# Optimization experiments

Hardware: AMD Instinct MI355X
Metric: run time of the kernel (lower is better)

The kernel has to match this reference:

```python
import jax, jax.numpy as jnp
import numpy as np

N = 10000
E = 160000
DIMS = [256, 256, 256, 256]
EPS = 1e-5
DSCALE = 1.0
SPE_IDX = 0


def setup_inputs() -> dict:
    key = jax.random.key(0)
    ks = jax.random.split(key, 40)
    inp = {}
    inp['x'] = jax.random.normal(ks[0], (N, DIMS[0]), dtype=jnp.float32)
    inp['src'] = jax.random.randint(ks[1], (E,), 0, N, dtype=jnp.int32)
    inp['dst'] = jax.random.randint(ks[2], (E,), 0, N, dtype=jnp.int32)
    k = 3
    for i, (din, dout) in enumerate(zip(DIMS[:-1], DIMS[1:])):
        s = 1.0 / np.sqrt(din)
        inp[f'Ws{i}'] = jax.random.uniform(ks[k], (din, dout), jnp.float32, -s, s); k += 1
        inp[f'Wn{i}'] = jax.random.uniform(ks[k], (din, dout), jnp.float32, -s, s); k += 1
        inp[f'b{i}'] = jnp.zeros((dout,), jnp.float32)
        inp[f'g{i}'] = jnp.ones((dout,), jnp.float32)
        inp[f'be{i}'] = jnp.zeros((dout,), jnp.float32)
    return inp


def _sage(h, src, dst, Ws, Wn, b):
    # mean aggregation over in-neighbors: segment-sum gathered src feats over dst
    agg = jax.ops.segment_sum(h[src], dst, num_segments=N)          # [N, din]
    deg = jax.ops.segment_sum(jnp.ones((E,), h.dtype), dst, num_segments=N)
    mean = agg / jnp.maximum(deg, 1.0)[:, None]
    return h @ Ws + mean @ Wn + b


def _bn(h, g, be):
    # BatchNorm1d, training mode (biased batch variance)
    mu = jnp.mean(h, axis=0)
    var = jnp.mean((h - mu) ** 2, axis=0)
    return (h - mu) * jax.lax.rsqrt(var + EPS) * g + be


def reference(x, src, dst, Ws0, Wn0, b0, g0, be0, Ws1, Wn1, b1, g1, be1,
              Ws2, Wn2, b2, g2, be2):
    params = [(Ws0, Wn0, b0, g0, be0), (Ws1, Wn1, b1, g1, be1),
              (Ws2, Wn2, b2, g2, be2)]
    n_layers = len(params)
    outs = x
    for i, (Ws, Wn, b, g, be) in enumerate(params):
        outs = _sage(outs, src, dst, Ws, Wn, b)
        # hid side-outputs (sigmoid(outs*dscale)[spe_idx]) don't affect outs path
        outs = _bn(outs, g, be)
        if i != n_layers - 1:
            outs = jax.nn.relu(outs)
        else:
            outs = jax.nn.sigmoid(outs)
    return outs
```

## Files before the change

### kernel.cpp

```cpp
#include <hip/hip_runtime.h>
#include <math.h>

#define NN 10000
#define EE 160000
#define DIM 256
#define KK 512
#define CAP 128
#define EPS_BN 1e-5f
#define AST 516

typedef __attribute__((ext_vector_type(8)))  short bf16x8;
typedef __attribute__((ext_vector_type(16))) float f32x16;

union U16 { uint2 u2[2]; bf16x8 v; };

static __device__ __forceinline__ unsigned short f2bf(float f) {
    unsigned u = __float_as_uint(f);
    unsigned r = (u + 0x7fffu + ((u >> 16) & 1u)) >> 16;
    return (unsigned short)r;
}
static __device__ __forceinline__ float bflo(unsigned v) { return __uint_as_float(v << 16); }
static __device__ __forceinline__ float bfhi(unsigned v) { return __uint_as_float(v & 0xffff0000u); }
static __device__ __forceinline__ unsigned packbf(float a, float b) {
    return (unsigned)f2bf(a) | ((unsigned)f2bf(b) << 16);
}

struct Params {
    const float* x; const int* src; const int* dst;
    const float *Ws0, *Wn0, *Ws1, *Wn1, *Ws2, *Wn2;
    const float *g0, *be0, *g1, *be1, *g2, *be2;
    float* out;
    unsigned short* hx;
    unsigned short* z0;
    unsigned short* z1;
    unsigned short* wcat;
    float* stats;
    int* cnt;
    int* slots;
};

static __device__ __forceinline__ void accum8(float* a, uint4 v) {
    a[0] += bflo(v.x); a[1] += bfhi(v.x);
    a[2] += bflo(v.y); a[3] += bfhi(v.y);
    a[4] += bflo(v.z); a[5] += bfhi(v.z);
    a[6] += bflo(v.w); a[7] += bfhi(v.w);
}
static __device__ __forceinline__ void accum8n(float* a, uint4 v,
                                               const float* sc, const float* sh) {
    a[0] += fmaxf(bflo(v.x) * sc[0] + sh[0], 0.f);
    a[1] += fmaxf(bfhi(v.x) * sc[1] + sh[1], 0.f);
    a[2] += fmaxf(bflo(v.y) * sc[2] + sh[2], 0.f);
    a[3] += fmaxf(bfhi(v.y) * sc[3] + sh[3], 0.f);
    a[4] += fmaxf(bflo(v.z) * sc[4] + sh[4], 0.f);
    a[5] += fmaxf(bfhi(v.z) * sc[5] + sh[5], 0.f);
    a[6] += fmaxf(bflo(v.w) * sc[6] + sh[6], 0.f);
    a[7] += fmaxf(bfhi(v.w) * sc[7] + sh[7], 0.f);
}

__global__ __launch_bounds__(256) void k_prep(Params P) {
    int g0 = blockIdx.x * 256 + threadIdx.x;
    int stride = gridDim.x * 256;
    for (int g = g0; g < NN * 64; g += stride) {
        int r = g >> 6, c4 = (g & 63) * 4;
        float4 v = *(const float4*)(P.x + (size_t)r * DIM + c4);
        uint2 p; p.x = packbf(v.x, v.y); p.y = packbf(v.z, v.w);
        *(uint2*)(P.hx + (size_t)r * DIM + c4) = p;
    }
    for (int g = g0; g < 3 * DIM * KK; g += stride) {
        int L = g >> 17; int i = g & 131071;
        int k = i >> 8, n = i & 255;
        const float* Ws = (L == 0) ? P.Ws0 : ((L == 1) ? P.Ws1 : P.Ws2);
        const float* Wn = (L == 0) ? P.Wn0 : ((L == 1) ? P.Wn1 : P.Wn2);
        float v = (k < DIM) ? Ws[(size_t)k * DIM + n] : Wn[(size_t)(k - DIM) * DIM + n];
        P.wcat[(size_t)L * DIM * KK + (size_t)n * KK + k] = f2bf(v);
    }
    for (int g = g0; g < NN + 6 * DIM; g += stride) {
        if (g < NN) P.cnt[g] = 0;
        else P.stats[g - NN] = 0.f;
    }
}

__global__ __launch_bounds__(256) void k_bucket(Params P) {
    int e = blockIdx.x * 256 + threadIdx.x;
    if (e < EE) {
        int d = P.dst[e];
        int p = atomicAdd(&P.cnt[d], 1);
        if (p < CAP) P.slots[(size_t)d * CAP + p] = P.src[e];
    }
}

__global__ __launch_bounds__(512) void k_ag(Params P, int L,
                                            const unsigned short* __restrict__ gsrc,
                                            unsigned short* __restrict__ gdst) {
    __shared__ unsigned short At[32][AST];
    int t = threadIdx.x;
    int wave = t >> 6, lane = t & 63;
    int h = lane >> 5, l = lane & 31;

    float sc[8], sh[8];
    if (L > 0) {
        const float* st = P.stats + (L - 1) * 2 * DIM;
        const float* gam = (L == 1) ? P.g0 : P.g1;
        const float* bet = (L == 1) ? P.be0 : P.be1;
#pragma unroll
        for (int i = 0; i < 8; ++i) {
            int c = l * 8 + i;
            float mu  = st[c] * (1.0f / NN);
            float var = st[DIM + c] * (1.0f / NN) - mu * mu;
            float k = rsqrtf(var + EPS_BN) * gam[c];
            sc[i] = k;
            sh[i] = bet[c] - mu * k;
        }
    }
    const uint4* srcm = (const uint4*)gsrc;

    for (int i = 0; i < 4; ++i) {
        int m = wave * 4 + i;
        int node = blockIdx.x * 32 + m;
        unsigned short* arow = &At[m][0];
        if (node >= NN) {
            if (h == 0) {
                uint2 z2 = make_uint2(0u, 0u);
                *(uint2*)(arow + l * 8)           = z2;
                *(uint2*)(arow + l * 8 + 4)       = z2;
                *(uint2*)(arow + 256 + l * 8)     = z2;
                *(uint2*)(arow + 256 + l * 8 + 4) = z2;
            }
            continue;
        }
        int cnt = P.cnt[node]; if (cnt > CAP) cnt = CAP;
        const int* sl = P.slots + (size_t)node * CAP;
        if (h == 0) {
            uint4 z = srcm[(size_t)node * 32 + l];
            uint4 o;
            if (L > 0) {
                o.x = packbf(fmaxf(bflo(z.x) * sc[0] + sh[0], 0.f),
                             fmaxf(bfhi(z.x) * sc[1] + sh[1], 0.f));
                o.y = packbf(fmaxf(bflo(z.y) * sc[2] + sh[2], 0.f),
                             fmaxf(bfhi(z.y) * sc[3] + sh[3], 0.f));
                o.z = packbf(fmaxf(bflo(z.z) * sc[4] + sh[4], 0.f),
                             fmaxf(bfhi(z.z) * sc[5] + sh[5], 0.f));
                o.w = packbf(fmaxf(bflo(z.w) * sc[6] + sh[6], 0.f),
                             fmaxf(bfhi(z.w) * sc[7] + sh[7], 0.f));
            } else o = z;
            *(uint2*)(arow + l * 8)     = make_uint2(o.x, o.y);
            *(uint2*)(arow + l * 8 + 4) = make_uint2(o.z, o.w);
        }
        float a[8] = {0, 0, 0, 0, 0, 0, 0, 0};
        int j = h;
        if (L == 0) {
            for (; j + 6 < cnt; j += 8) {
                uint4 v0 = srcm[(size_t)sl[j + 0] * 32 + l];
                uint4 v1 = srcm[(size_t)sl[j + 2] * 32 + l];
                uint4 v2 = srcm[(size_t)sl[j + 4] * 32 + l];
                uint4 v3 = srcm[(size_t)sl[j + 6] * 32 + l];
                accum8(a, v0); accum8(a, v1); accum8(a, v2); accum8(a, v3);
            }
            for (; j < cnt; j += 2) accum8(a, srcm[(size_t)sl[j] * 32 + l]);
        } else {
            for (; j + 6 < cnt; j += 8) {
                uint4 v0 = srcm[(size_t)sl[j + 0] * 32 + l];
                uint4 v1 = srcm[(size_t)sl[j + 2] * 32 + l];
                uint4 v2 = srcm[(size_t)sl[j + 4] * 32 + l];
                uint4 v3 = srcm[(size_t)sl[j + 6] * 32 + l];
                accum8n(a, v0, sc, sh); accum8n(a, v1, sc, sh);
                accum8n(a, v2, sc, sh); accum8n(a, v3, sc, sh);
            }
            for (; j < cnt; j += 2) accum8n(a, srcm[(size_t)sl[j] * 32 + l], sc, sh);
        }
#pragma unroll
        for (int q = 0; q < 8; ++q) a[q] += __shfl_xor(a[q], 32);
        if (h == 0) {
            float inv = 1.0f / (float)(cnt > 1 ? cnt : 1);
            *(uint2*)(arow + 256 + l * 8)     = make_uint2(packbf(a[0] * inv, a[1] * inv),
                                                           packbf(a[2] * inv, a[3] * inv));
            *(uint2*)(arow + 256 + l * 8 + 4) = make_uint2(packbf(a[4] * inv, a[5] * inv),
                                                           packbf(a[6] * inv, a[7] * inv));
        }
    }
    __syncthreads();

    const unsigned short* wcatL = P.wcat + (size_t)L * DIM * KK;
    float* statsL = P.stats + L * 2 * DIM;
    int m = l;
    int row0 = blockIdx.x * 32;
    int colw0 = wave * 32;
    const unsigned short* Bp = wcatL + (size_t)(colw0 + m) * KK + h * 8;
    const unsigned short* Arow = &At[m][0];
    f32x16 acc;
#pragma unroll
    for (int i = 0; i < 16; ++i) acc[i] = 0.f;
#pragma unroll 8
    for (int k0 = 0; k0 < KK; k0 += 16) {
        U16 ua;
        ua.u2[0] = *(const uint2*)(Arow + k0 + h * 8);
        ua.u2[1] = *(const uint2*)(Arow + k0 + h * 8 + 4);
        bf16x8 av = ua.v;
        bf16x8 bv = *(const bf16x8*)(Bp + k0);
        acc = __builtin_amdgcn_mfma_f32_32x32x16_bf16(av, bv, acc, 0, 0, 0);
    }
    int cc = colw0 + m;
    float s = 0.f, s2 = 0.f;
#pragma unroll
    for (int reg = 0; reg < 16; ++reg) {
        int r = row0 + (reg & 3) + 8 * (reg >> 2) + 4 * h;
        if (r < NN) {
            float v = acc[reg];
            gdst[(size_t)r * DIM + cc] = f2bf(v);
            s += v; s2 += v * v;
        }
    }
    s  += __shfl_down(s, 32);
    s2 += __shfl_down(s2, 32);
    if (h == 0) {
        atomicAdd(&statsL[cc], s);
        atomicAdd(&statsL[DIM + cc], s2);
    }
}

__global__ __launch_bounds__(256) void k_norm(Params P) {
    const float* statsL = P.stats + 2 * 2 * DIM;
    int t = threadIdx.x;
    int c8 = (t & 31) * 8;
    int r = blockIdx.x * 8 + (t >> 5);
    float sc[8], sh[8];
#pragma unroll
    for (int i = 0; i < 8; ++i) {
        int c = c8 + i;
        float mu  = statsL[c] * (1.0f / NN);
        float var = statsL[DIM + c] * (1.0f / NN) - mu * mu;
        float k = rsqrtf(var + EPS_BN) * P.g2[c];
        sc[i] = k;
        sh[i] = P.be2[c] - mu * k;
    }
    uint4 v = *(const uint4*)(P.z0 + (size_t)r * DIM + c8);
    float f[8] = {bflo(v.x), bfhi(v.x), bflo(v.y), bfhi(v.y),
                  bflo(v.z), bfhi(v.z), bflo(v.w), bfhi(v.w)};
#pragma unroll
    for (int i = 0; i < 8; ++i) f[i] = f[i] * sc[i] + sh[i];
    float4 o0, o1;
    o0.x = 1.0f / (1.0f + __expf(-f[0]));
    o0.y = 1.0f / (1.0f + __expf(-f[1]));
    o0.z = 1.0f / (1.0f + __expf(-f[2]));
    o0.w = 1.0f / (1.0f + __expf(-f[3]));
    o1.x = 1.0f / (1.0f + __expf(-f[4]));
    o1.y = 1.0f / (1.0f + __expf(-f[5]));
    o1.z = 1.0f / (1.0f + __expf(-f[6]));
    o1.w = 1.0f / (1.0f + __expf(-f[7]));
    *(float4*)(P.out + (size_t)r * DIM + c8)     = o0;
    *(float4*)(P.out + (size_t)r * DIM + c8 + 4) = o1;
}

extern "C" void kernel_launch(void* const* d_in, const int* in_sizes, int n_in,
                              void* d_out, int out_size, void* d_ws, size_t ws_size,
                              hipStream_t stream) {
    Params P;
    P.x   = (const float*)d_in[0];
    P.src = (const int*)d_in[1];
    P.dst = (const int*)d_in[2];
    P.Ws0 = (const float*)d_in[3];  P.Wn0 = (const float*)d_in[4];
    P.g0  = (const float*)d_in[6];  P.be0 = (const float*)d_in[7];
    P.Ws1 = (const float*)d_in[8];  P.Wn1 = (const float*)d_in[9];
    P.g1  = (const float*)d_in[11]; P.be1 = (const float*)d_in[12];
    P.Ws2 = (const float*)d_in[13]; P.Wn2 = (const float*)d_in[14];
    P.g2  = (const float*)d_in[16]; P.be2 = (const float*)d_in[17];
    P.out = (float*)d_out;

    char* ws = (char*)d_ws;
    size_t off = 0;
    P.hx   = (unsigned short*)(ws + off); off += (size_t)NN * DIM * 2;
    P.z0   = (unsigned short*)(ws + off); off += (size_t)NN * DIM * 2;
    P.z1   = (unsigned short*)(ws + off); off += (size_t)NN * DIM * 2;
    P.wcat = (unsigned short*)(ws + off); off += (size_t)3 * DIM * KK * 2;
    P.stats = (float*)(ws + off); off += 3 * 2 * DIM * sizeof(float);
    P.cnt   = (int*)(ws + off); off += (size_t)NN * 4; off = (off + 255) & ~(size_t)255;
    P.slots = (int*)(ws + off); off += (size_t)NN * CAP * 4;
    (void)ws_size;

    k_prep<<<512, 256, 0, stream>>>(P);
    k_bucket<<<(EE + 255) / 256, 256, 0, stream>>>(P);
    k_ag<<<313, 512, 0, stream>>>(P, 0, P.hx, P.z0);
    k_ag<<<313, 512, 0, stream>>>(P, 1, P.z0, P.z1);
    k_ag<<<313, 512, 0, stream>>>(P, 2, P.z1, P.z0);
    k_norm<<<NN / 8, 256, 0, stream>>>(P);
}
```

Baseline: 223.2 us.

## Halve aggregation tile to 16 rows using 16x16x32 MFMA and double grid

Each aggregation/GEMM block now handles 16 nodes instead of 32 and launches 626 blocks instead of 313. This is meant to fill the GPU's CUs more evenly and raise occupancy, with a launch-bounds occupancy hint added. The MFMA switches from 32x32x16 to two 16x16x32 instructions per wave, and the BN-stat reduction is reworked to match. The slot capacity per destination is also cut from 128 to 64, which shrinks the bucket buffer but drops more neighbors if a node's in-degree is high. Weight tiles are now re-read by twice as many blocks.

```diff
diff --git a/kernel.cpp b/kernel.cpp
--- a/kernel.cpp
+++ b/kernel.cpp
@@ -5,12 +5,12 @@
 #define EE 160000
 #define DIM 256
 #define KK 512
-#define CAP 128
+#define CAP 64
 #define EPS_BN 1e-5f
 #define AST 516
 
 typedef __attribute__((ext_vector_type(8)))  short bf16x8;
-typedef __attribute__((ext_vector_type(16))) float f32x16;
+typedef __attribute__((ext_vector_type(4)))  float f32x4;
 
 union U16 { uint2 u2[2]; bf16x8 v; };
 
@@ -89,10 +89,10 @@
     }
 }
 
-__global__ __launch_bounds__(512) void k_ag(Params P, int L,
-                                            const unsigned short* __restrict__ gsrc,
-                                            unsigned short* __restrict__ gdst) {
-    __shared__ unsigned short At[32][AST];
+__global__ __launch_bounds__(512, 4) void k_ag(Params P, int L,
+                                               const unsigned short* __restrict__ gsrc,
+                                               unsigned short* __restrict__ gdst) {
+    __shared__ unsigned short At[16][AST];
     int t = threadIdx.x;
     int wave = t >> 6, lane = t & 63;
     int h = lane >> 5, l = lane & 31;
@@ -114,9 +114,9 @@
     }
     const uint4* srcm = (const uint4*)gsrc;
 
-    for (int i = 0; i < 4; ++i) {
-        int m = wave * 4 + i;
-        int node = blockIdx.x * 32 + m;
+    for (int i = 0; i < 2; ++i) {
+        int m = wave * 2 + i;
+        int node = blockIdx.x * 16 + m;
         unsigned short* arow = &At[m][0];
         if (node >= NN) {
             if (h == 0) {
@@ -182,39 +182,49 @@
 
     const unsigned short* wcatL = P.wcat + (size_t)L * DIM * KK;
     float* statsL = P.stats + L * 2 * DIM;
-    int m = l;
-    int row0 = blockIdx.x * 32;
-    int colw0 = wave * 32;
-    const unsigned short* Bp = wcatL + (size_t)(colw0 + m) * KK + h * 8;
-    const unsigned short* Arow = &At[m][0];
-    f32x16 acc;
-#pragma unroll
-    for (int i = 0; i < 16; ++i) acc[i] = 0.f;
+    int m16 = lane & 15, g = lane >> 4;
+    int row0 = blockIdx.x * 16;
+    int n0 = wave * 32;
+    const unsigned short* Arow = &At[m16][0];
+    const unsigned short* Bp0 = wcatL + (size_t)(n0 + m16) * KK + g * 8;
+    const unsigned short* Bp1 = Bp0 + (size_t)16 * KK;
+    f32x4 acc0, acc1;
+#pragma unroll
+    for (int i = 0; i < 4; ++i) { acc0[i] = 0.f; acc1[i] = 0.f; }
 #pragma unroll 8
-    for (int k0 = 0; k0 < KK; k0 += 16) {
+    for (int k0 = 0; k0 < KK; k0 += 32) {
         U16 ua;
-        ua.u2[0] = *(const uint2*)(Arow + k0 + h * 8);
-        ua.u2[1] = *(const uint2*)(Arow + k0 + h * 8 + 4);
+        ua.u2[0] = *(const uint2*)(Arow + k0 + g * 8);
+        ua.u2[1] = *(const uint2*)(Arow + k0 + g * 8 + 4);
         bf16x8 av = ua.v;
-        bf16x8 bv = *(const bf16x8*)(Bp + k0);
-        acc = __builtin_amdgcn_mfma_f32_32x32x16_bf16(av, bv, acc, 0, 0, 0);
-    }
-    int cc = colw0 + m;
-    float s = 0.f, s2 = 0.f;
-#pragma unroll
-    for (int reg = 0; reg < 16; ++reg) {
-        int r = row0 + (reg & 3) + 8 * (reg >> 2) + 4 * h;
+        bf16x8 bv0 = *(const bf16x8*)(Bp0 + k0);
+        bf16x8 bv1 = *(const bf16x8*)(Bp1 + k0);
+        acc0 = __builtin_amdgcn_mfma_f32_16x16x32_bf16(av, bv0, acc0, 0, 0, 0);
+        acc1 = __builtin_amdgcn_mfma_f32_16x16x32_bf16(av, bv1, acc1, 0, 0, 0);
+    }
+    int c0 = n0 + m16, c1 = c0 + 16;
+    float s0 = 0.f, s20 = 0.f, s1 = 0.f, s21 = 0.f;
+#pragma unroll
+    for (int reg = 0; reg < 4; ++reg) {
+        int r = row0 + g * 4 + reg;
         if (r < NN) {
-            float v = acc[reg];
-            gdst[(size_t)r * DIM + cc] = f2bf(v);
-            s += v; s2 += v * v;
-        }
-    }
-    s  += __shfl_down(s, 32);
-    s2 += __shfl_down(s2, 32);
-    if (h == 0) {
-        atomicAdd(&statsL[cc], s);
-        atomicAdd(&statsL[DIM + cc], s2);
+            float v0 = acc0[reg];
+            gdst[(size_t)r * DIM + c0] = f2bf(v0);
+            s0 += v0; s20 += v0 * v0;
+            float v1 = acc1[reg];
+            gdst[(size_t)r * DIM + c1] = f2bf(v1);
+            s1 += v1; s21 += v1 * v1;
+        }
+    }
+    s0  += __shfl_xor(s0, 16);  s0  += __shfl_xor(s0, 32);
+    s20 += __shfl_xor(s20, 16); s20 += __shfl_xor(s20, 32);
+    s1  += __shfl_xor(s1, 16);  s1  += __shfl_xor(s1, 32);
+    s21 += __shfl_xor(s21, 16); s21 += __shfl_xor(s21, 32);
+    if (g == 0) {
+        atomicAdd(&statsL[c0], s0);
+        atomicAdd(&statsL[DIM + c0], s20);
+        atomicAdd(&statsL[c1], s1);
+        atomicAdd(&statsL[DIM + c1], s21);
     }
 }
 
@@ -279,8 +289,8 @@
 
     k_prep<<<512, 256, 0, stream>>>(P);
     k_bucket<<<(EE + 255) / 256, 256, 0, stream>>>(P);
-    k_ag<<<313, 512, 0, stream>>>(P, 0, P.hx, P.z0);
-    k_ag<<<313, 512, 0, stream>>>(P, 1, P.z0, P.z1);
-    k_ag<<<313, 512, 0, stream>>>(P, 2, P.z1, P.z0);
+    k_ag<<<626, 512, 0, stream>>>(P, 0, P.hx, P.z0);
+    k_ag<<<626, 512, 0, stream>>>(P, 1, P.z0, P.z1);
+    k_ag<<<626, 512, 0, stream>>>(P, 2, P.z1, P.z0);
     k_norm<<<NN / 8, 256, 0, stream>>>(P);
 }
```

Result: slower. 255.7 us (+14.6%).

## Preload neighbor slots into registers and broadcast via shuffles in aggregation

Applied to the files above, without the earlier changes.

Each wave now loads its four nodes' counts, neighbor slot lists (one slot per lane) and self features up front, then broadcasts neighbor indices with wave shuffles instead of reading the slot array from global memory inside the gather loop. The gather loop is unrolled to eight outstanding loads per half-wave. CAP drops from 128 to 64 so a 64-lane wave can hold the whole list, and launch bounds request two blocks per CU. This is meant to cut dependent index-load latency and raise memory-level parallelism. It risks more register pressure and silently truncates any node with more than 64 in-edges.

```diff
diff --git a/kernel.cpp b/kernel.cpp
--- a/kernel.cpp
+++ b/kernel.cpp
@@ -5,7 +5,7 @@
 #define EE 160000
 #define DIM 256
 #define KK 512
-#define CAP 128
+#define CAP 64
 #define EPS_BN 1e-5f
 #define AST 516
 
@@ -89,9 +89,9 @@
     }
 }
 
-__global__ __launch_bounds__(512) void k_ag(Params P, int L,
-                                            const unsigned short* __restrict__ gsrc,
-                                            unsigned short* __restrict__ gdst) {
+__global__ __launch_bounds__(512, 2) void k_ag(Params P, int L,
+                                               const unsigned short* __restrict__ gsrc,
+                                               unsigned short* __restrict__ gdst) {
     __shared__ unsigned short At[32][AST];
     int t = threadIdx.x;
     int wave = t >> 6, lane = t & 63;
@@ -114,9 +114,22 @@
     }
     const uint4* srcm = (const uint4*)gsrc;
 
+    int node0 = blockIdx.x * 32 + wave * 4;
+    int4 c4 = *(const int4*)(P.cnt + node0);
+    int cs[4] = {c4.x, c4.y, c4.z, c4.w};
+    int slv[4];
+    uint4 own[4];
+#pragma unroll
+    for (int i = 0; i < 4; ++i) {
+        int node = node0 + i;
+        int nc = (node < NN) ? node : (NN - 1);
+        slv[i] = P.slots[(size_t)nc * CAP + lane];
+        own[i] = srcm[(size_t)nc * 32 + l];
+    }
+#pragma unroll
     for (int i = 0; i < 4; ++i) {
         int m = wave * 4 + i;
-        int node = blockIdx.x * 32 + m;
+        int node = node0 + i;
         unsigned short* arow = &At[m][0];
         if (node >= NN) {
             if (h == 0) {
@@ -128,10 +141,10 @@
             }
             continue;
         }
-        int cnt = P.cnt[node]; if (cnt > CAP) cnt = CAP;
-        const int* sl = P.slots + (size_t)node * CAP;
+        int cnt = cs[i]; if (cnt > CAP) cnt = CAP;
+        int sv = slv[i];
         if (h == 0) {
-            uint4 z = srcm[(size_t)node * 32 + l];
+            uint4 z = own[i];
             uint4 o;
             if (L > 0) {
                 o.x = packbf(fmaxf(bflo(z.x) * sc[0] + sh[0], 0.f),
@@ -147,26 +160,48 @@
             *(uint2*)(arow + l * 8 + 4) = make_uint2(o.z, o.w);
         }
         float a[8] = {0, 0, 0, 0, 0, 0, 0, 0};
-        int j = h;
-        if (L == 0) {
-            for (; j + 6 < cnt; j += 8) {
-                uint4 v0 = srcm[(size_t)sl[j + 0] * 32 + l];
-                uint4 v1 = srcm[(size_t)sl[j + 2] * 32 + l];
-                uint4 v2 = srcm[(size_t)sl[j + 4] * 32 + l];
-                uint4 v3 = srcm[(size_t)sl[j + 6] * 32 + l];
+        int j = 0;
+        for (; j + 15 < cnt; j += 16) {
+            int r0 = __shfl(sv, j +  0 + h), r1 = __shfl(sv, j +  2 + h);
+            int r2 = __shfl(sv, j +  4 + h), r3 = __shfl(sv, j +  6 + h);
+            int r4 = __shfl(sv, j +  8 + h), r5 = __shfl(sv, j + 10 + h);
+            int r6 = __shfl(sv, j + 12 + h), r7 = __shfl(sv, j + 14 + h);
+            uint4 v0 = srcm[(size_t)r0 * 32 + l];
+            uint4 v1 = srcm[(size_t)r1 * 32 + l];
+            uint4 v2 = srcm[(size_t)r2 * 32 + l];
+            uint4 v3 = srcm[(size_t)r3 * 32 + l];
+            uint4 v4 = srcm[(size_t)r4 * 32 + l];
+            uint4 v5 = srcm[(size_t)r5 * 32 + l];
+            uint4 v6 = srcm[(size_t)r6 * 32 + l];
+            uint4 v7 = srcm[(size_t)r7 * 32 + l];
+            if (L == 0) {
                 accum8(a, v0); accum8(a, v1); accum8(a, v2); accum8(a, v3);
-            }
-            for (; j < cnt; j += 2) accum8(a, srcm[(size_t)sl[j] * 32 + l]);
-        } else {
-            for (; j + 6 < cnt; j += 8) {
-                uint4 v0 = srcm[(size_t)sl[j + 0] * 32 + l];
-                uint4 v1 = srcm[(size_t)sl[j + 2] * 32 + l];
-                uint4 v2 = srcm[(size_t)sl[j + 4] * 32 + l];
-                uint4 v3 = srcm[(size_t)sl[j + 6] * 32 + l];
+                accum8(a, v4); accum8(a, v5); accum8(a, v6); accum8(a, v7);
+            } else {
                 accum8n(a, v0, sc, sh); accum8n(a, v1, sc, sh);
                 accum8n(a, v2, sc, sh); accum8n(a, v3, sc, sh);
+                accum8n(a, v4, sc, sh); accum8n(a, v5, sc, sh);
+                accum8n(a, v6, sc, sh); accum8n(a, v7, sc, sh);
             }
-            for (; j < cnt; j += 2) accum8n(a, srcm[(size_t)sl[j] * 32 + l], sc, sh);
+        }
+        for (; j + 3 < cnt; j += 4) {
+            int r0 = __shfl(sv, j + h), r1 = __shfl(sv, j + 2 + h);
+            uint4 v0 = srcm[(size_t)r0 * 32 + l];
+            uint4 v1 = srcm[(size_t)r1 * 32 + l];
+            if (L == 0) { accum8(a, v0); accum8(a, v1); }
+            else { accum8n(a, v0, sc, sh); accum8n(a, v1, sc, sh); }
+        }
+        for (; j + 1 < cnt; j += 2) {
+            int r0 = __shfl(sv, j + h);
+            uint4 v0 = srcm[(size_t)r0 * 32 + l];
+            if (L == 0) accum8(a, v0); else accum8n(a, v0, sc, sh);
+        }
+        if (j < cnt) {
+            int r0 = __shfl(sv, cnt - 1);
+            uint4 v0 = srcm[(size_t)r0 * 32 + l];
+            if (h == 0) {
+                if (L == 0) accum8(a, v0); else accum8n(a, v0, sc, sh);
+            }
         }
 #pragma unroll
         for (int q = 0; q < 8; ++q) a[q] += __shfl_xor(a[q], 32);
```

Result: slower. 249.7 us (+11.9%).
